# Kernel optimization log

Hardware: AMD Instinct MI355X
Metric: run time of the kernel (lower is better)

Reference implementation:

```python
import jax, jax.numpy as jnp
import numpy as np

L = 16384; ENC = 64; DMODEL = 256; DSTATE = 64; DCONV = 4; EXPAND = 2
NLAYERS = 3; NCLASSES = 11
DIN = EXPAND * DMODEL                 # 512
HEADDIM = 64
NHEADS = DIN // HEADDIM               # 8
DXBC = DIN + 2 * DSTATE               # 640 (ngroups=1)
DPROJ = 2 * DIN + 2 * DSTATE + NHEADS # 1160
NDIR = 6
ORDERS = [(0, 1, 2), (0, 2, 1), (1, 0, 2), (1, 2, 0), (2, 0, 1), (2, 1, 0)]
SCALES = [1, 2, 4]
EPS = 1e-5


def setup_inputs() -> dict:
    key = jax.random.key(0)
    ks = iter(jax.random.split(key, 64))
    def nrm(shape, s=0.02):
        return jax.random.normal(next(ks), shape, jnp.float32) * s
    S = len(SCALES)
    return {
        "vec_real": jax.random.normal(next(ks), (L, ENC), jnp.float32),
        "vec_imag": jax.random.normal(next(ks), (L, ENC), jnp.float32),
        "coords": jax.random.randint(next(ks), (L, 4), 0, 128, jnp.int32),
        # input projection (Linear 128->256, LayerNorm)
        "inp_w": nrm((2 * ENC, DMODEL)), "inp_b": jnp.zeros((DMODEL,)),
        "inp_ln_w": jnp.ones((DMODEL,)), "inp_ln_b": jnp.zeros((DMODEL,)),
        # shared Mamba2 blocks, stacked over NLAYERS
        "ln_w": jnp.ones((NLAYERS, DMODEL)), "ln_b": jnp.zeros((NLAYERS, DMODEL)),
        "in_proj_w": nrm((NLAYERS, DMODEL, DPROJ)),
        "conv_w": nrm((NLAYERS, DXBC, DCONV), 0.1), "conv_b": jnp.zeros((NLAYERS, DXBC)),
        "dt_bias": nrm((NLAYERS, NHEADS), 0.5),
        "A_log": jnp.log(jnp.broadcast_to(jnp.arange(1, NHEADS + 1, dtype=jnp.float32), (NLAYERS, NHEADS))),
        "Dskip": jnp.ones((NLAYERS, NHEADS)),
        "rms_w": jnp.ones((NLAYERS, DIN)),
        "out_proj_w": nrm((NLAYERS, DIN, DMODEL)),
        # fusion MLP
        "fus_ln_w": jnp.ones((NDIR * DMODEL,)), "fus_ln_b": jnp.zeros((NDIR * DMODEL,)),
        "fus_w": nrm((NDIR * DMODEL, DMODEL)), "fus_b": jnp.zeros((DMODEL,)),
        # classifier
        "cls_ln_w": jnp.ones((S * DMODEL,)), "cls_ln_b": jnp.zeros((S * DMODEL,)),
        "cls_w1": nrm((S * DMODEL, 2 * DMODEL)), "cls_b1": jnp.zeros((2 * DMODEL,)),
        "cls_w2": nrm((2 * DMODEL, DMODEL)), "cls_b2": jnp.zeros((DMODEL,)),
        "cls_w3": nrm((DMODEL, NCLASSES)), "cls_b3": jnp.zeros((NCLASSES,)),
    }


def layer_norm(x, w, b):
    mu = x.mean(-1, keepdims=True)
    v = ((x - mu) ** 2).mean(-1, keepdims=True)
    return (x - mu) * jax.lax.rsqrt(v + EPS) * w + b


def mamba2(x, in_proj_w, conv_w, conv_b, dt_bias, A_log, Dskip, rms_w, out_proj_w):
    # x: [B, L, DMODEL]
    Bsz, Ls, _ = x.shape
    zxbcdt = x @ in_proj_w                                  # [B,L,DPROJ]
    z, xBC, dt = jnp.split(zxbcdt, [DIN, DIN + DXBC], axis=-1)
    dt = jax.nn.softplus(dt + dt_bias)                      # [B,L,H]
    # causal depthwise conv1d over xBC, then SiLU
    xc = jnp.transpose(xBC, (0, 2, 1))                      # [B,C,L]
    xc = jax.lax.conv_general_dilated(xc, conv_w[:, None, :], (1,), [(DCONV - 1, 0)],
                                      feature_group_count=DXBC)
    xBC = jax.nn.silu(jnp.transpose(xc, (0, 2, 1)) + conv_b)
    xs, Bm, Cm = jnp.split(xBC, [DIN, DIN + DSTATE], axis=-1)
    xs = xs.reshape(Bsz, Ls, NHEADS, HEADDIM)               # [B,L,H,P]
    A = -jnp.exp(A_log)                                     # [H]

    def step(state, inp):
        x_t, B_t, C_t, dt_t = inp                           # [B,H,P],[B,S],[B,S],[B,H]
        dA = jnp.exp(dt_t * A)                              # [B,H]
        state = state * dA[..., None, None] + (dt_t[..., None, None]
                 * x_t[..., :, None] * B_t[:, None, None, :])
        y = jnp.einsum('bhps,bs->bhp', state, C_t)
        return state, y

    init = jnp.zeros((Bsz, NHEADS, HEADDIM, DSTATE), x.dtype)
    seq = (jnp.moveaxis(xs, 1, 0), jnp.moveaxis(Bm, 1, 0),
           jnp.moveaxis(Cm, 1, 0), jnp.moveaxis(dt, 1, 0))
    _, ys = jax.lax.scan(step, init, seq)                   # [L,B,H,P]
    y = jnp.moveaxis(ys, 0, 1) + Dskip[None, None, :, None] * xs
    y = y.reshape(Bsz, Ls, DIN)
    # gated RMSNorm (norm_before_gate=False)
    y = y * jax.nn.silu(z)
    y = y * jax.lax.rsqrt((y * y).mean(-1, keepdims=True) + EPS) * rms_w
    return y @ out_proj_w


def reference(vec_real, vec_imag, coords, inp_w, inp_b, inp_ln_w, inp_ln_b,
              ln_w, ln_b, in_proj_w, conv_w, conv_b, dt_bias, A_log, Dskip,
              rms_w, out_proj_w, fus_ln_w, fus_ln_b, fus_w, fus_b,
              cls_ln_w, cls_ln_b, cls_w1, cls_b1, cls_w2, cls_b2, cls_w3, cls_b3):
    x = jnp.concatenate([vec_real, vec_imag], -1)           # [L,128]
    h = layer_norm(x @ inp_w + inp_b, inp_ln_w, inp_ln_b)
    h = jax.nn.gelu(h, approximate=False)                   # [L,D]
    # 6 traversal orders via lexsort (np.lexsort semantics: last key primary)
    perms = [jnp.lexsort(tuple(coords[:, a] for a in reversed(axes))) for axes in ORDERS]
    perm = jnp.stack(perms)                                 # [6,L]
    inv = jnp.argsort(perm, axis=1)                         # [6,L]
    xs = h[perm]                                            # [6,L,D] (directions as batch, shared weights)

    def layer_step(xcur, p):
        lw, lb, ipw, cw, cb, dtb, al, dk, rw, ow = p
        y = mamba2(layer_norm(xcur, lw, lb), ipw, cw, cb, dtb, al, dk, rw, ow)
        return xcur + y, None

    params = (ln_w, ln_b, in_proj_w, conv_w, conv_b, dt_bias, A_log, Dskip, rms_w, out_proj_w)
    xs, _ = jax.lax.scan(layer_step, xs, params)
    restored = jnp.take_along_axis(xs, inv[:, :, None], axis=1)  # [6,L,D]
    multi = jnp.transpose(restored, (1, 0, 2)).reshape(L, NDIR * DMODEL)
    fused = layer_norm(multi, fus_ln_w, fus_ln_b) @ fus_w + fus_b
    fused = jax.nn.gelu(fused, approximate=False)           # [L,D]
    # multi-scale pooling; L divisible by every scale -> equal windows
    pooled = jnp.concatenate([fused.reshape(s, L // s, DMODEL).mean(1).mean(0)
                              for s in SCALES], 0)          # [3*D]
    hc = layer_norm(pooled, cls_ln_w, cls_ln_b)
    hc = jax.nn.gelu(hc @ cls_w1 + cls_b1, approximate=False)
    hc = jax.nn.gelu(hc @ cls_w2 + cls_b2, approximate=False)
    return hc @ cls_w3 + cls_b3                             # [NCLASSES]
```

## Files before the change

### kernel.cpp

```cpp
#include <hip/hip_runtime.h>
#include <hip/hip_bf16.h>
#include <math.h>

#define LSEQ 16384
#define NC 128

using short8  = __attribute__((ext_vector_type(8))) short;
using floatx4 = __attribute__((ext_vector_type(4))) float;

__device__ __forceinline__ float bf2f(ushort u){ union{unsigned u; float f;} x; x.u = ((unsigned)u)<<16; return x.f; }
__device__ __forceinline__ ushort f2bf(float f){ union{float f; unsigned u;} x; x.f=f; unsigned u=x.u; return (ushort)((u + 0x7FFFu + ((u>>16)&1u)) >> 16); }
__device__ __forceinline__ float geluf(float x){ return 0.5f*x*(1.f+erff(x*0.70710678118654752f)); }
__device__ __forceinline__ float siluf(float x){ return x/(1.f+__expf(-x)); }
__device__ __forceinline__ float softplusf(float x){ return x>20.f ? x : log1pf(__expf(x)); }

__device__ __forceinline__ float blockSum256(float v, float* red){
  int t = threadIdx.x;
  red[t]=v; __syncthreads();
  #pragma unroll
  for (int s=128;s>0;s>>=1){ if (t<s) red[t]+=red[t+s]; __syncthreads(); }
  float r = red[0]; __syncthreads();
  return r;
}

__device__ const int ORD[6][3] = {{0,1,2},{0,2,1},{1,0,2},{1,2,0},{2,0,1},{2,1,0}};

__global__ __launch_bounds__(256) void zrank_k(int* __restrict__ rank){
  rank[blockIdx.x*256 + threadIdx.x] = 0;
}

__global__ __launch_bounds__(256) void sortp_k(const int* __restrict__ coords, int* __restrict__ rank){
  __shared__ unsigned long long sk[256];
  int d = blockIdx.y; int tid = threadIdx.x;
  int a0=ORD[d][0], a1=ORD[d][1], a2=ORD[d][2];
  int ibase = blockIdx.x*1024;
  int jbase = blockIdx.z*4096;
  unsigned long long mykey[4]; int rk[4] = {0,0,0,0};
  #pragma unroll
  for (int r=0;r<4;++r){
    int i = ibase + r*256 + tid;
    unsigned k3 = ((unsigned)coords[i*4+a0]<<14) | ((unsigned)coords[i*4+a1]<<7) | (unsigned)coords[i*4+a2];
    mykey[r] = (((unsigned long long)k3)<<14) | (unsigned)i;
  }
  for (int j0=jbase; j0<jbase+4096; j0+=256){
    int j = j0 + tid;
    unsigned j3 = ((unsigned)coords[j*4+a0]<<14) | ((unsigned)coords[j*4+a1]<<7) | (unsigned)coords[j*4+a2];
    sk[tid] = (((unsigned long long)j3)<<14) | (unsigned)j;
    __syncthreads();
    #pragma unroll 8
    for (int jj=0; jj<256; ++jj){
      unsigned long long kj = sk[jj];
      #pragma unroll
      for (int r=0;r<4;++r) rk[r] += (kj < mykey[r]) ? 1 : 0;
    }
    __syncthreads();
  }
  #pragma unroll
  for (int r=0;r<4;++r)
    atomicAdd(&rank[d*LSEQ + ibase + r*256 + tid], rk[r]);
}

__global__ __launch_bounds__(256) void sfin_k(const int* __restrict__ rank, int* __restrict__ perm, int* __restrict__ inv){
  int g = blockIdx.x*256 + threadIdx.x;
  int d = g >> 14, i = g & 16383;
  int r = rank[g];
  perm[d*LSEQ + r] = i;
  inv[g] = r;
}

__global__ __launch_bounds__(256) void concat_k(const float* __restrict__ vr, const float* __restrict__ vi, float* __restrict__ xcat){
  int idx = blockIdx.x*256 + threadIdx.x;
  int i = idx >> 7, c = idx & 127;
  xcat[idx] = (c<64) ? vr[(i<<6)+c] : vi[(i<<6)+c-64];
}

__global__ __launch_bounds__(256) void tr_k(const float* __restrict__ in, ushort* __restrict__ out, int K, int N){
  __shared__ float tile[32][33];
  int tx = threadIdx.x & 31, ty = threadIdx.x >> 5;
  int k0 = blockIdx.y*32, n0 = blockIdx.x*32;
  #pragma unroll
  for (int q=0;q<4;++q){
    int k = k0 + ty + q*8, n = n0 + tx;
    if (k < K && n < N) tile[ty+q*8][tx] = in[(size_t)k*N + n];
  }
  __syncthreads();
  #pragma unroll
  for (int q=0;q<4;++q){
    int n = n0 + ty + q*8, k = k0 + tx;
    if (n < N && k < K) out[(size_t)n*K + k] = f2bf(tile[tx][ty+q*8]);
  }
}

template<int EPI, bool AF32>
__global__ __launch_bounds__(256) void gemm_bf_k(
  const void* __restrict__ Ain, int lda, const ushort* __restrict__ Bt,
  int N, int K, float* __restrict__ of,
  const float* __restrict__ bias, const float* __restrict__ rrow)
{
  __shared__ __align__(16) ushort As[64*32];
  __shared__ __align__(16) ushort Bs[64*32];
  int tid = threadIdx.x;
  int n0 = blockIdx.x*64, m0 = blockIdx.y*64;
  int w = tid>>6, lane = tid&63;
  int wm = (w>>1)*32, wn = (w&1)*32;
  int sr = tid>>2, skk = (tid&3)*8;
  floatx4 acc[2][2] = {};
  for (int k0=0; k0<K; k0+=32){
    if constexpr (AF32){
      const float* A = (const float*)Ain;
      float4 v0 = *(const float4*)(A + (size_t)(m0+sr)*lda + k0 + skk);
      float4 v1 = *(const float4*)(A + (size_t)(m0+sr)*lda + k0 + skk + 4);
      ushort o[8] = {f2bf(v0.x),f2bf(v0.y),f2bf(v0.z),f2bf(v0.w),f2bf(v1.x),f2bf(v1.y),f2bf(v1.z),f2bf(v1.w)};
      *(uint4*)(&As[sr*32+skk]) = *(uint4*)o;
    } else {
      const ushort* A = (const ushort*)Ain;
      *(uint4*)(&As[sr*32+skk]) = *(const uint4*)(A + (size_t)(m0+sr)*lda + k0 + skk);
    }
    uint4 bv = make_uint4(0u,0u,0u,0u);
    if (n0+sr < N) bv = *(const uint4*)(Bt + (size_t)(n0+sr)*K + k0 + skk);
    *(uint4*)(&Bs[sr*32+skk]) = bv;
    __syncthreads();
    int kq = lane>>4, l16 = lane&15;
    short8 bf0 = *(const short8*)(&Bs[(wn      + l16)*32 + kq*8]);
    short8 bf1 = *(const short8*)(&Bs[(wn + 16 + l16)*32 + kq*8]);
    #pragma unroll
    for (int ti=0; ti<2; ++ti){
      short8 af = *(const short8*)(&As[(wm + ti*16 + l16)*32 + kq*8]);
      acc[ti][0] = __builtin_amdgcn_mfma_f32_16x16x32_bf16(af, bf0, acc[ti][0], 0,0,0);
      acc[ti][1] = __builtin_amdgcn_mfma_f32_16x16x32_bf16(af, bf1, acc[ti][1], 0,0,0);
    }
    __syncthreads();
  }
  int l16 = lane&15, lq = lane>>4;
  #pragma unroll
  for (int ti=0; ti<2; ++ti)
  #pragma unroll
  for (int tj=0; tj<2; ++tj)
  #pragma unroll
  for (int r=0; r<4; ++r){
    int row = m0 + wm + ti*16 + lq*4 + r;
    int col = n0 + wn + tj*16 + l16;
    if (col >= N) continue;
    float v = acc[ti][tj][r];
    of[(size_t)row*N + col] = v + bias[col];
  }
}

template<int KC, int EPI>
__global__ __launch_bounds__(256) void gemmNS_k(
  const ushort* __restrict__ A, int lda, const ushort* __restrict__ Bt,
  float* __restrict__ of, const float* __restrict__ bias, const float* __restrict__ rrow)
{
  __shared__ __align__(16) ushort As[64*264];
  __shared__ __align__(16) ushort Bs[64*32];
  const int K = KC*256;
  int tid = threadIdx.x;
  int m0 = blockIdx.x*64;
  int w = tid>>6, lane = tid&63;
  int wm = (w>>1)*32, wn = (w&1)*32;
  int sr = tid>>2, skk = (tid&3)*8;
  int l16 = lane&15, kq = lane>>4;
  floatx4 acc[4][2][2] = {};
  for (int kb=0; kb<KC; ++kb){
    #pragma unroll
    for (int ki=0;ki<8;++ki)
      *(uint4*)(&As[sr*264 + ki*32 + skk]) = *(const uint4*)(A + (size_t)(m0+sr)*lda + kb*256 + ki*32 + skk);
    __syncthreads();
    for (int nt=0; nt<4; ++nt){
      for (int k0=0; k0<256; k0+=32){
        *(uint4*)(&Bs[sr*32+skk]) = *(const uint4*)(Bt + (size_t)(nt*64+sr)*K + kb*256 + k0 + skk);
        __syncthreads();
        short8 bf0 = *(const short8*)(&Bs[(wn      + l16)*32 + kq*8]);
        short8 bf1 = *(const short8*)(&Bs[(wn + 16 + l16)*32 + kq*8]);
        #pragma unroll
        for (int ti=0; ti<2; ++ti){
          short8 af = *(const short8*)(&As[(wm + ti*16 + l16)*264 + k0 + kq*8]);
          acc[nt][ti][0] = __builtin_amdgcn_mfma_f32_16x16x32_bf16(af, bf0, acc[nt][ti][0], 0,0,0);
          acc[nt][ti][1] = __builtin_amdgcn_mfma_f32_16x16x32_bf16(af, bf1, acc[nt][ti][1], 0,0,0);
        }
        __syncthreads();
      }
    }
  }
  #pragma unroll
  for (int nt=0; nt<4; ++nt)
  #pragma unroll
  for (int ti=0; ti<2; ++ti)
  #pragma unroll
  for (int tj=0; tj<2; ++tj)
  #pragma unroll
  for (int r=0; r<4; ++r){
    int row = m0 + wm + ti*16 + kq*4 + r;
    int col = nt*64 + wn + tj*16 + l16;
    float v = acc[nt][ti][tj][r];
    if (EPI==2) of[(size_t)row*256 + col] += v * rrow[row];
    else        of[(size_t)row*256 + col] = geluf(v + bias[col]);
  }
}

__global__ __launch_bounds__(256) void gemm1_k(
  const float* __restrict__ xs,
  const float* __restrict__ lnw, const float* __restrict__ lnb,
  const ushort* __restrict__ Wt,
  ushort* __restrict__ xbc, float* __restrict__ odt, const float* __restrict__ dtb)
{
  __shared__ __align__(16) ushort As[64*264];
  __shared__ __align__(16) ushort Bs[64*32];
  int tid = threadIdx.x;
  int m0 = blockIdx.x*64;
  int w = tid>>6, lane = tid&63;
  int wm = (w>>1)*32, wn = (w&1)*32;
  int sr = tid>>2, skk = (tid&3)*8;
  int l16 = lane&15, kq = lane>>4;
  float va[8][8];
  float s = 0.f, s2 = 0.f;
  const float* rowp = xs + (size_t)(m0+sr)*256;
  #pragma unroll
  for (int ki=0;ki<8;++ki){
    float4 v0 = *(const float4*)(rowp + ki*32 + skk);
    float4 v1 = *(const float4*)(rowp + ki*32 + skk + 4);
    va[ki][0]=v0.x; va[ki][1]=v0.y; va[ki][2]=v0.z; va[ki][3]=v0.w;
    va[ki][4]=v1.x; va[ki][5]=v1.y; va[ki][6]=v1.z; va[ki][7]=v1.w;
    #pragma unroll
    for (int j=0;j<8;++j){ s += va[ki][j]; s2 += va[ki][j]*va[ki][j]; }
  }
  s  += __shfl_xor(s,1,64);  s  += __shfl_xor(s,2,64);
  s2 += __shfl_xor(s2,1,64); s2 += __shfl_xor(s2,2,64);
  float mu = s*(1.f/256.f);
  float var = s2*(1.f/256.f) - mu*mu;
  float rs = rsqrtf(fmaxf(var,0.f)+1e-5f);
  #pragma unroll
  for (int ki=0;ki<8;++ki){
    ushort o[8];
    #pragma unroll
    for (int j=0;j<8;++j) o[j] = f2bf((va[ki][j]-mu)*rs*lnw[ki*32+skk+j] + lnb[ki*32+skk+j]);
    *(uint4*)(&As[sr*264 + ki*32 + skk]) = *(uint4*)o;
  }
  __syncthreads();
  for (int nt=0; nt<11; ++nt){
    floatx4 acc[2][2] = {};
    for (int k0=0; k0<256; k0+=32){
      int nr = 512 + nt*64 + sr;
      uint4 bv = make_uint4(0u,0u,0u,0u);
      if (nr < 1160) bv = *(const uint4*)(Wt + (size_t)nr*256 + k0 + skk);
      *(uint4*)(&Bs[sr*32+skk]) = bv;
      __syncthreads();
      short8 bf0 = *(const short8*)(&Bs[(wn      + l16)*32 + kq*8]);
      short8 bf1 = *(const short8*)(&Bs[(wn + 16 + l16)*32 + kq*8]);
      #pragma unroll
      for (int ti=0; ti<2; ++ti){
        short8 af = *(const short8*)(&As[(wm + ti*16 + l16)*264 + k0 + kq*8]);
        acc[ti][0] = __builtin_amdgcn_mfma_f32_16x16x32_bf16(af, bf0, acc[ti][0], 0,0,0);
        acc[ti][1] = __builtin_amdgcn_mfma_f32_16x16x32_bf16(af, bf1, acc[ti][1], 0,0,0);
      }
      __syncthreads();
    }
    #pragma unroll
    for (int ti=0; ti<2; ++ti)
    #pragma unroll
    for (int tj=0; tj<2; ++tj)
    #pragma unroll
    for (int r=0; r<4; ++r){
      int row = m0 + wm + ti*16 + kq*4 + r;
      int col = nt*64 + wn + tj*16 + l16;
      float v = acc[ti][tj][r];
      if (col < 640) xbc[(size_t)row*640 + col] = f2bf(v);
      else if (col < 648) odt[(size_t)row*8 + (col-640)] = softplusf(v + dtb[col-640]);
    }
  }
}

__global__ __launch_bounds__(256) void ln_gelu_k(const float* __restrict__ in, float* __restrict__ out,
    const float* __restrict__ w, const float* __restrict__ b){
  __shared__ float red[256];
  int t = threadIdx.x; size_t base = (size_t)blockIdx.x*256;
  float v = in[base+t];
  float mu = blockSum256(v, red) * (1.f/256.f);
  float dv = v - mu;
  float var = blockSum256(dv*dv, red) * (1.f/256.f);
  float rs = rsqrtf(var + 1e-5f);
  out[base+t] = geluf(dv*rs*w[t] + b[t]);
}

__global__ __launch_bounds__(256) void scatter_k(const float* __restrict__ h, const int* __restrict__ perm, float* __restrict__ xs){
  int blk = blockIdx.x;
  int t = threadIdx.x;
  int d = blk >> 14; int r = blk & 16383;
  int src = perm[d*LSEQ + r];
  xs[(size_t)blk*256 + t] = h[(size_t)src*256 + t];
}

__global__ __launch_bounds__(256) void bnd_k(const ushort* __restrict__ xbc, ushort* __restrict__ bnd){
  int b = blockIdx.x;
  int d = b / NC, c = b % NC;
  size_t row0 = (size_t)d*LSEQ + (size_t)c*128;
  for (int idx = threadIdx.x; idx < 3*640; idx += 256){
    int j = idx/640;
    ushort v = (c==0) ? (ushort)0 : xbc[(row0 - 3 + j)*640 + (idx - j*640)];
    bnd[(size_t)b*3*640 + idx] = v;
  }
}

__global__ __launch_bounds__(256) void conv_k(ushort* __restrict__ xbc, const ushort* __restrict__ bnd,
    const float* __restrict__ convw, const float* __restrict__ convb){
  int b = blockIdx.x;
  int d = b / NC, c = b % NC;
  size_t row0 = (size_t)d*LSEQ + (size_t)c*128;
  int tid = threadIdx.x;
  for (int s0 = tid; s0 < 640; s0 += 256){
    float w0=convw[s0*4], w1=convw[s0*4+1], w2=convw[s0*4+2], w3=convw[s0*4+3];
    float cb=convb[s0];
    float h0=0.f,h1=0.f,h2=0.f;
    if (c != 0){
      const ushort* bp = bnd + (size_t)b*3*640;
      h0=bf2f(bp[s0]); h1=bf2f(bp[640+s0]); h2=bf2f(bp[1280+s0]);
    }
    ushort* p = xbc + row0*640 + s0;
    for (int r=0;r<128;++r){
      float cur = bf2f(*p);
      *p = f2bf(siluf(cb + w0*h0 + w1*h1 + w2*h2 + w3*cur));
      h0=h1; h1=h2; h2=cur;
      p += 640;
    }
  }
}

__global__ __launch_bounds__(256) void ssd_dstate_k(
  const ushort* __restrict__ xbc, const float* __restrict__ dtf, const float* __restrict__ alog,
  ushort* __restrict__ dsb, float* __restrict__ gam, int dh0)
{
  int c = blockIdx.x, dhg = blockIdx.y;
  int dh = dh0 + dhg;
  int d = dh >> 3, h = dh & 7;
  int tid = threadIdx.x;
  float Ah = -__expf(alog[h]);
  __shared__ __align__(16) ushort XT[64*136];
  __shared__ __align__(16) ushort BwT[64*136];
  __shared__ float sdt[128];
  __shared__ float scs[128];
  size_t row0 = (size_t)d*LSEQ + (size_t)c*128;
  if (tid < 128){
    float v = dtf[(row0+tid)*8 + h];
    sdt[tid] = v;
    float x = v;
    #pragma unroll
    for (int o=1;o<64;o<<=1){ float t = __shfl_up(x,(unsigned)o,64); if ((tid&63)>=o) x += t; }
    scs[tid] = x;
  }
  __syncthreads();
  if (tid>=64 && tid<128) scs[tid] += scs[63];
  __syncthreads();
// ... 180 lines not shown
  }
  #pragma unroll
  for (int mt=0; mt<2; ++mt)
  #pragma unroll
  for (int nt=0; nt<4; ++nt)
  #pragma unroll
  for (int r=0; r<4; ++r){
    int tl = w*32 + mt*16 + kq*4 + r;
    int p  = nt*16 + l16;
    float xv = bf2f(XT[p*136 + tl]);
    float yv = Y[mt][nt][r] + Dv*xv;
    xbc[(row0 + tl)*640 + h*64 + p] = f2bf(yv);
  }
}

__global__ __launch_bounds__(512) void scan_legacy_k(ushort* __restrict__ xbc, const float* __restrict__ dtf,
  const float* __restrict__ convw, const float* __restrict__ convb,
  const float* __restrict__ alog, const float* __restrict__ dskip)
{
  int d = blockIdx.x >> 3, h = blockIdx.x & 7;
  int tid = threadIdx.x, p = tid & 63, sg = tid >> 6;
  float Ah = -__expf(alog[h]);
  float Dv = dskip[h];
  __shared__ float raw[19][192];
  __shared__ float cw[192][4];
  __shared__ float cb[192];
  __shared__ float sxc[16][192];
  __shared__ float sdt[16];
  __shared__ float sy[16][8][64];
  for (int c = tid; c < 192; c += 512){
    int ch = (c<64) ? h*64+c : (c<128 ? 512+(c-64) : 576+(c-128));
    #pragma unroll
    for (int k=0;k<4;++k) cw[c][k] = convw[ch*4+k];
    cb[c] = convb[ch];
  }
  for (int idx = tid; idx < 3*192; idx += 512) raw[idx/192][idx%192] = 0.f;
  float st[8];
  #pragma unroll
  for (int j=0;j<8;++j) st[j]=0.f;
  size_t rowbase = (size_t)d*LSEQ;
  __syncthreads();
  for (int t0=0; t0<LSEQ; t0+=16){
    for (int idx = tid; idx < 16*192; idx += 512){
      int tt = idx/192, c = idx%192;
      int ch = (c<64) ? h*64+c : (c<128 ? 512+(c-64) : 576+(c-128));
      raw[3+tt][c] = bf2f(xbc[(rowbase + t0 + tt)*640 + ch]);
    }
    if (tid < 16) sdt[tid] = dtf[(rowbase + t0 + tid)*8 + h];
    __syncthreads();
    for (int idx = tid; idx < 16*192; idx += 512){
      int tt = idx/192, c = idx%192;
      float v = cb[c] + cw[c][0]*raw[tt][c] + cw[c][1]*raw[tt+1][c]
                      + cw[c][2]*raw[tt+2][c] + cw[c][3]*raw[tt+3][c];
      sxc[tt][c] = siluf(v);
    }
    __syncthreads();
    for (int tt=0; tt<16; ++tt){
      float dtv = sdt[tt];
      float dA = __expf(dtv*Ah);
      float xb = dtv * sxc[tt][p];
      float Bl[8], Cl[8];
      #pragma unroll
      for (int q=0;q<2;++q){
        *(floatx4*)&Bl[q*4] = *(const floatx4*)&sxc[tt][64  + sg*8 + q*4];
        *(floatx4*)&Cl[q*4] = *(const floatx4*)&sxc[tt][128 + sg*8 + q*4];
      }
      float part = 0.f;
      #pragma unroll
      for (int j=0;j<8;++j){ st[j] = st[j]*dA + xb*Bl[j]; part += st[j]*Cl[j]; }
      sy[tt][sg][p] = part;
    }
    __syncthreads();
    for (int idx = tid; idx < 16*64; idx += 512){
      int tt = idx>>6, pp = idx&63;
      float yv = sy[tt][0][pp]+sy[tt][1][pp]+sy[tt][2][pp]+sy[tt][3][pp]
               + sy[tt][4][pp]+sy[tt][5][pp]+sy[tt][6][pp]+sy[tt][7][pp] + Dv*sxc[tt][pp];
      xbc[(rowbase + t0 + tt)*640 + h*64 + pp] = f2bf(yv);
    }
    for (int idx = tid; idx < 3*192; idx += 512){
      int r = idx/192, c = idx%192;
      raw[r][c] = raw[16+r][c];
    }
    __syncthreads();
  }
}

__global__ __launch_bounds__(256) void zgate_k(
  const float* __restrict__ xs,
  const float* __restrict__ lnw, const float* __restrict__ lnb,
  const ushort* __restrict__ Wzt, ushort* __restrict__ xbc,
  const float* __restrict__ rmsw, float* __restrict__ rrg)
{
  __shared__ __align__(16) ushort As[64*264];
  __shared__ __align__(16) ushort Bs[64*32];
  __shared__ float gsum[64*32];
  int tid = threadIdx.x;
  int m0 = blockIdx.x*64;
  int w = tid>>6, lane = tid&63;
  int wm = (w>>1)*32, wn = (w&1)*32;
  int sr = tid>>2, skk = (tid&3)*8;
  int l16 = lane&15, kq = lane>>4;
  float va[8][8];
  float s = 0.f, s2 = 0.f;
  const float* rowp = xs + (size_t)(m0+sr)*256;
  #pragma unroll
  for (int ki=0;ki<8;++ki){
    float4 v0 = *(const float4*)(rowp + ki*32 + skk);
    float4 v1 = *(const float4*)(rowp + ki*32 + skk + 4);
    va[ki][0]=v0.x; va[ki][1]=v0.y; va[ki][2]=v0.z; va[ki][3]=v0.w;
    va[ki][4]=v1.x; va[ki][5]=v1.y; va[ki][6]=v1.z; va[ki][7]=v1.w;
    #pragma unroll
    for (int j=0;j<8;++j){ s += va[ki][j]; s2 += va[ki][j]*va[ki][j]; }
  }
  s  += __shfl_xor(s,1,64);  s  += __shfl_xor(s,2,64);
  s2 += __shfl_xor(s2,1,64); s2 += __shfl_xor(s2,2,64);
  float mu = s*(1.f/256.f);
  float var = s2*(1.f/256.f) - mu*mu;
  float rs = rsqrtf(fmaxf(var,0.f)+1e-5f);
  #pragma unroll
  for (int ki=0;ki<8;++ki){
    ushort o[8];
    #pragma unroll
    for (int j=0;j<8;++j) o[j] = f2bf((va[ki][j]-mu)*rs*lnw[ki*32+skk+j] + lnb[ki*32+skk+j]);
    *(uint4*)(&As[sr*264 + ki*32 + skk]) = *(uint4*)o;
  }
  float racc[2][4] = {};
  __syncthreads();
  for (int nt=0; nt<8; ++nt){
    floatx4 acc[2][2] = {};
    for (int k0=0; k0<256; k0+=32){
      uint4 bv = *(const uint4*)(Wzt + (size_t)(nt*64 + sr)*256 + k0 + skk);
      *(uint4*)(&Bs[sr*32+skk]) = bv;
      __syncthreads();
      short8 bf0 = *(const short8*)(&Bs[(wn      + l16)*32 + kq*8]);
      short8 bf1 = *(const short8*)(&Bs[(wn + 16 + l16)*32 + kq*8]);
      #pragma unroll
      for (int ti=0; ti<2; ++ti){
        short8 af = *(const short8*)(&As[(wm + ti*16 + l16)*264 + k0 + kq*8]);
        acc[ti][0] = __builtin_amdgcn_mfma_f32_16x16x32_bf16(af, bf0, acc[ti][0], 0,0,0);
        acc[ti][1] = __builtin_amdgcn_mfma_f32_16x16x32_bf16(af, bf1, acc[ti][1], 0,0,0);
      }
      __syncthreads();
    }
    #pragma unroll
    for (int ti=0; ti<2; ++ti)
    #pragma unroll
    for (int tj=0; tj<2; ++tj)
    #pragma unroll
    for (int r=0; r<4; ++r){
      int row = m0 + wm + ti*16 + kq*4 + r;
      int col = nt*64 + wn + tj*16 + l16;
      float z = acc[ti][tj][r];
      float y = bf2f(xbc[(size_t)row*640 + col]);
      float g = y * siluf(z);
      racc[ti][r] += g*g;
      xbc[(size_t)row*640 + col] = f2bf(g * rmsw[col]);
    }
  }
  #pragma unroll
  for (int ti=0; ti<2; ++ti)
  #pragma unroll
  for (int r=0; r<4; ++r)
    gsum[(wm + ti*16 + kq*4 + r)*32 + (w&1)*16 + l16] = racc[ti][r];
  __syncthreads();
  if (tid < 64){
    float s0 = 0.f;
    #pragma unroll 8
    for (int cc=0;cc<32;++cc) s0 += gsum[tid*32+cc];
    rrg[m0+tid] = rsqrtf(s0*(1.f/512.f) + 1e-5f);
  }
}

__global__ __launch_bounds__(256) void fuse_ln_k(const float* __restrict__ xs, const int* __restrict__ inv,
    const float* __restrict__ w, const float* __restrict__ b, ushort* __restrict__ out){
  __shared__ float red[256];
  int i = blockIdx.x, t = threadIdx.x;
  float v[6];
  float s = 0.f;
  #pragma unroll
  for (int d=0; d<6; ++d){
    int r = inv[d*LSEQ + i];
    v[d] = xs[((size_t)d*LSEQ + r)*256 + t];
    s += v[d];
  }
  float mu = blockSum256(s, red) * (1.f/1536.f);
  float s2 = 0.f;
  #pragma unroll
  for (int d=0; d<6; ++d){ float dv = v[d]-mu; s2 += dv*dv; }
  float var = blockSum256(s2, red) * (1.f/1536.f);
  float rs = rsqrtf(var + 1e-5f);
  #pragma unroll
  for (int d=0; d<6; ++d){
    int c = d*256 + t;
    out[(size_t)i*1536 + c] = f2bf((v[d]-mu)*rs*w[c] + b[c]);
  }
}

__global__ void zero_k(float* p){ p[threadIdx.x] = 0.f; }

__global__ __launch_bounds__(256) void pool_k(const float* __restrict__ fused, float* __restrict__ pooled){
  int t = threadIdx.x;
  size_t r0 = (size_t)blockIdx.x*256;
  float s = 0.f;
  for (int r=0;r<256;++r) s += fused[(r0+r)*256 + t];
  atomicAdd(&pooled[t], s);
}

__global__ __launch_bounds__(256) void cls_k(const float* __restrict__ pooled,
  const float* __restrict__ lnw, const float* __restrict__ lnb,
  const float* __restrict__ w1, const float* __restrict__ b1,
  const float* __restrict__ w2, const float* __restrict__ b2,
  const float* __restrict__ w3, const float* __restrict__ b3, float* __restrict__ out)
{
  __shared__ float red[256];
  __shared__ float hcn[768]; __shared__ float h1[512]; __shared__ float h2[256];
  int t = threadIdx.x;
  float m = pooled[t] * (1.f/16384.f);
  float mu = blockSum256(m, red) * (1.f/256.f);
  float dv = m - mu;
  float var = blockSum256(dv*dv, red) * (1.f/256.f);
  float rs = rsqrtf(var + 1e-5f);
  #pragma unroll
  for (int rep=0; rep<3; ++rep){
    int c = rep*256 + t;
    hcn[c] = dv*rs*lnw[c] + lnb[c];
  }
  __syncthreads();
  for (int n=t; n<512; n+=256){
    float a = b1[n];
    for (int c=0;c<768;++c) a += hcn[c]*w1[c*512+n];
    h1[n] = geluf(a);
  }
  __syncthreads();
  {
    float a = b2[t];
    for (int c=0;c<512;++c) a += h1[c]*w2[c*256+t];
    h2[t] = geluf(a);
  }
  __syncthreads();
  if (t<11){
    float a = b3[t];
    for (int c=0;c<256;++c) a += h2[c]*w3[c*11+t];
    out[t] = a;
  }
}

extern "C" void kernel_launch(void* const* d_in, const int* in_sizes, int n_in,
                              void* d_out, int out_size, void* d_ws, size_t ws_size,
                              hipStream_t stream)
{
  const float* vec_real = (const float*)d_in[0];
  const float* vec_imag = (const float*)d_in[1];
  const int*   coords   = (const int*)d_in[2];
  const float* inp_w    = (const float*)d_in[3];
  const float* inp_b    = (const float*)d_in[4];
  const float* inp_ln_w = (const float*)d_in[5];
  const float* inp_ln_b = (const float*)d_in[6];
  const float* ln_w     = (const float*)d_in[7];
  const float* ln_b     = (const float*)d_in[8];
  const float* in_proj_w= (const float*)d_in[9];
  const float* conv_w   = (const float*)d_in[10];
  const float* conv_b   = (const float*)d_in[11];
  const float* dt_bias  = (const float*)d_in[12];
  const float* A_log    = (const float*)d_in[13];
  const float* Dskip    = (const float*)d_in[14];
  const float* rms_w    = (const float*)d_in[15];
  const float* out_proj_w=(const float*)d_in[16];
  const float* fus_ln_w = (const float*)d_in[17];
  const float* fus_ln_b = (const float*)d_in[18];
  const float* fus_w    = (const float*)d_in[19];
  const float* fus_b    = (const float*)d_in[20];
  const float* cls_ln_w = (const float*)d_in[21];
  const float* cls_ln_b = (const float*)d_in[22];
  const float* cls_w1   = (const float*)d_in[23];
  const float* cls_b1   = (const float*)d_in[24];
  const float* cls_w2   = (const float*)d_in[25];
  const float* cls_b2   = (const float*)d_in[26];
  const float* cls_w3   = (const float*)d_in[27];
  const float* cls_b3   = (const float*)d_in[28];
  (void)in_sizes; (void)n_in; (void)out_size;

  char* ws = (char*)d_ws;
  size_t off = 0;
  auto alloc = [&](size_t bytes)->char* { char* p = ws + off; off = (off + bytes + 255) & ~(size_t)255; return p; };
  int*    perm  = (int*)alloc((size_t)6*LSEQ*4);
  int*    inv   = (int*)alloc((size_t)6*LSEQ*4);
  float*  xs    = (float*)alloc((size_t)6*LSEQ*256*4);
  ushort* xbc   = (ushort*)alloc((size_t)6*LSEQ*640*2);
  float*  dtfb  = (float*)alloc((size_t)6*LSEQ*8*4);
  float*  rrg   = (float*)alloc((size_t)6*LSEQ*4);
  ushort* wtr   = (ushort*)alloc((size_t)1536*256*2);
  float*  pooled= (float*)alloc(256*4);
  size_t base_off = off;
  if (base_off > ws_size) return;

  float* gam = (float*)((char*)wtr + 600*1024);
  int* rankb = (int*)rrg;

  const size_t BND_SZ = (size_t)6*NC*3*640*2;
  size_t dsb_off = base_off + ((BND_SZ + 255) & ~(size_t)255);
  ushort* bndb = (ushort*)(ws + base_off);
  ushort* dsb  = (ushort*)(ws + dsb_off);
  long long avail2 = (long long)ws_size - (long long)dsb_off;
  int gsize = 0;
  const int cands[10] = {48,24,16,12,8,6,4,3,2,1};
  for (int ci=0; ci<10; ++ci){
    if ((long long)((size_t)cands[ci]*NC*4096*2 + 512) <= avail2){ gsize = cands[ci]; break; }
  }

  float*  xcat = (float*)((char*)xbc + 0);
  float*  tmpF = (float*)((char*)xbc + (16u<<20));
  float*  hbuf = (float*)((char*)xbc + (48u<<20));
  ushort* multiB = (ushort*)((char*)xbc + 0);
  float*  fused  = (float*)((char*)xbc + (100u<<20));

  dim3 b256(256);
  zrank_k<<<dim3(6*LSEQ/256),b256,0,stream>>>(rankb);
  sortp_k<<<dim3(16,6,4),b256,0,stream>>>(coords, rankb);
  sfin_k<<<dim3(6*LSEQ/256),b256,0,stream>>>(rankb, perm, inv);
  concat_k<<<dim3(LSEQ*128/256),b256,0,stream>>>(vec_real, vec_imag, xcat);
  tr_k<<<dim3(8,4),b256,0,stream>>>(inp_w, wtr, 128, 256);
  gemm_bf_k<0,true><<<dim3(4, LSEQ/64),b256,0,stream>>>(xcat, 128, wtr, 256, 128, tmpF, inp_b, nullptr);
  ln_gelu_k<<<dim3(LSEQ),b256,0,stream>>>(tmpF, hbuf, inp_ln_w, inp_ln_b);
  scatter_k<<<dim3(6*LSEQ),b256,0,stream>>>(hbuf, perm, xs);

  for (int l=0;l<3;++l){
    const float* cwp = conv_w + (size_t)l*640*4;
    const float* cbp = conv_b + (size_t)l*640;
    const float* alp = A_log + l*8;
    const float* dkp = Dskip + l*8;
    tr_k<<<dim3(37,8),b256,0,stream>>>(in_proj_w + (size_t)l*256*1160, wtr, 256, 1160);
    gemm1_k<<<dim3(6*LSEQ/64),b256,0,stream>>>(xs, ln_w + l*256, ln_b + l*256,
        wtr, xbc, dtfb, dt_bias + l*8);
    if (gsize > 0){
      bnd_k<<<dim3(6*NC),b256,0,stream>>>(xbc, bndb);
      conv_k<<<dim3(6*NC),b256,0,stream>>>(xbc, bndb, cwp, cbp);
      for (int dh0=0; dh0<48; dh0+=gsize){
        ssd_dstate_k<<<dim3(NC,gsize),b256,0,stream>>>(xbc, dtfb, alp, dsb, gam, dh0);
        ssd_scan_k<<<dim3(gsize,2),b256,0,stream>>>(dsb, gam, dh0);
        ssd_out_k<<<dim3(NC,gsize),b256,0,stream>>>(xbc, dsb, dtfb, alp, dkp, dh0);
      }
    } else {
      scan_legacy_k<<<dim3(48),dim3(512),0,stream>>>(xbc, dtfb, cwp, cbp, alp, dkp);
    }
    zgate_k<<<dim3(6*LSEQ/64),b256,0,stream>>>(xs, ln_w + l*256, ln_b + l*256,
        wtr, xbc, rms_w + l*512, rrg);
    tr_k<<<dim3(8,16),b256,0,stream>>>(out_proj_w + (size_t)l*512*256, wtr, 512, 256);
    gemmNS_k<2,2><<<dim3(6*LSEQ/64),b256,0,stream>>>(xbc, 640, wtr, xs, nullptr, rrg);
  }

  fuse_ln_k<<<dim3(LSEQ),b256,0,stream>>>(xs, inv, fus_ln_w, fus_ln_b, multiB);
  tr_k<<<dim3(8,48),b256,0,stream>>>(fus_w, wtr, 1536, 256);
  gemmNS_k<6,3><<<dim3(LSEQ/64),b256,0,stream>>>(multiB, 1536, wtr, fused, fus_b, nullptr);
  zero_k<<<dim3(1),b256,0,stream>>>(pooled);
  pool_k<<<dim3(64),b256,0,stream>>>(fused, pooled);
  cls_k<<<dim3(1),b256,0,stream>>>(pooled, cls_ln_w, cls_ln_b, cls_w1, cls_b1, cls_w2, cls_b2, cls_w3, cls_b3, (float*)d_out);
}
```

Baseline: 3.119 ms.

## Keep GEMM A operands in registers and load B directly, dropping LDS staging

The in_proj, z-gate and NS GEMM kernels now hold LayerNorm'd or bf16 A fragments in registers and read B fragments straight from global memory. This removes the LDS tiles and the per-k-step __syncthreads barriers. The sort-rank kernel's j-range is also split across twice as many blocks to expose more parallelism. The trade-off is higher register pressure and LayerNorm statistics recomputed per lane group, and B loads are no longer shared across waves through LDS, so they may not coalesce as well.

```diff
diff --git a/kernel.cpp b/kernel.cpp
--- a/kernel.cpp
+++ b/kernel.cpp
@@ -34,7 +34,7 @@
   int d = blockIdx.y; int tid = threadIdx.x;
   int a0=ORD[d][0], a1=ORD[d][1], a2=ORD[d][2];
   int ibase = blockIdx.x*1024;
-  int jbase = blockIdx.z*4096;
+  int jbase = blockIdx.z*2048;
   unsigned long long mykey[4]; int rk[4] = {0,0,0,0};
   #pragma unroll
   for (int r=0;r<4;++r){
@@ -42,7 +42,7 @@
     unsigned k3 = ((unsigned)coords[i*4+a0]<<14) | ((unsigned)coords[i*4+a1]<<7) | (unsigned)coords[i*4+a2];
     mykey[r] = (((unsigned long long)k3)<<14) | (unsigned)i;
   }
-  for (int j0=jbase; j0<jbase+4096; j0+=256){
+  for (int j0=jbase; j0<jbase+2048; j0+=256){
     int j = j0 + tid;
     unsigned j3 = ((unsigned)coords[j*4+a0]<<14) | ((unsigned)coords[j*4+a1]<<7) | (unsigned)coords[j*4+a2];
     sk[tid] = (((unsigned long long)j3)<<14) | (unsigned)j;
@@ -91,11 +91,9 @@
   }
 }
 
-template<int EPI, bool AF32>
-__global__ __launch_bounds__(256) void gemm_bf_k(
-  const void* __restrict__ Ain, int lda, const ushort* __restrict__ Bt,
-  int N, int K, float* __restrict__ of,
-  const float* __restrict__ bias, const float* __restrict__ rrow)
+__global__ __launch_bounds__(256) void gemm0_k(
+  const float* __restrict__ A, int lda, const ushort* __restrict__ Bt,
+  int N, int K, float* __restrict__ of, const float* __restrict__ bias)
 {
   __shared__ __align__(16) ushort As[64*32];
   __shared__ __align__(16) ushort Bs[64*32];
@@ -106,16 +104,10 @@
   int sr = tid>>2, skk = (tid&3)*8;
   floatx4 acc[2][2] = {};
   for (int k0=0; k0<K; k0+=32){
-    if constexpr (AF32){
-      const float* A = (const float*)Ain;
-      float4 v0 = *(const float4*)(A + (size_t)(m0+sr)*lda + k0 + skk);
-      float4 v1 = *(const float4*)(A + (size_t)(m0+sr)*lda + k0 + skk + 4);
-      ushort o[8] = {f2bf(v0.x),f2bf(v0.y),f2bf(v0.z),f2bf(v0.w),f2bf(v1.x),f2bf(v1.y),f2bf(v1.z),f2bf(v1.w)};
-      *(uint4*)(&As[sr*32+skk]) = *(uint4*)o;
-    } else {
-      const ushort* A = (const ushort*)Ain;
-      *(uint4*)(&As[sr*32+skk]) = *(const uint4*)(A + (size_t)(m0+sr)*lda + k0 + skk);
-    }
+    float4 v0 = *(const float4*)(A + (size_t)(m0+sr)*lda + k0 + skk);
+    float4 v1 = *(const float4*)(A + (size_t)(m0+sr)*lda + k0 + skk + 4);
+    ushort o[8] = {f2bf(v0.x),f2bf(v0.y),f2bf(v0.z),f2bf(v0.w),f2bf(v1.x),f2bf(v1.y),f2bf(v1.z),f2bf(v1.w)};
+    *(uint4*)(&As[sr*32+skk]) = *(uint4*)o;
     uint4 bv = make_uint4(0u,0u,0u,0u);
     if (n0+sr < N) bv = *(const uint4*)(Bt + (size_t)(n0+sr)*K + k0 + skk);
     *(uint4*)(&Bs[sr*32+skk]) = bv;
@@ -141,8 +133,142 @@
     int row = m0 + wm + ti*16 + lq*4 + r;
     int col = n0 + wn + tj*16 + l16;
     if (col >= N) continue;
-    float v = acc[ti][tj][r];
-    of[(size_t)row*N + col] = v + bias[col];
+    of[(size_t)row*N + col] = acc[ti][tj][r] + bias[col];
+  }
+}
+
+__device__ __forceinline__ void ln_frags(const float* __restrict__ xs, int row,
+    const float* __restrict__ lnw, const float* __restrict__ lnb, int kq, short8 afr[8])
+{
+  const float* rowp = xs + (size_t)row*256;
+  float v[64];
+  float s=0.f, s2=0.f;
+  #pragma unroll
+  for (int kc=0;kc<8;++kc){
+    float4 a0 = *(const float4*)(rowp + kc*32 + kq*8);
+    float4 a1 = *(const float4*)(rowp + kc*32 + kq*8 + 4);
+    v[kc*8+0]=a0.x; v[kc*8+1]=a0.y; v[kc*8+2]=a0.z; v[kc*8+3]=a0.w;
+    v[kc*8+4]=a1.x; v[kc*8+5]=a1.y; v[kc*8+6]=a1.z; v[kc*8+7]=a1.w;
+  }
+  #pragma unroll
+  for (int j=0;j<64;++j){ s += v[j]; s2 += v[j]*v[j]; }
+  s  += __shfl_xor(s,16,64);  s  += __shfl_xor(s,32,64);
+  s2 += __shfl_xor(s2,16,64); s2 += __shfl_xor(s2,32,64);
+  float mu = s*(1.f/256.f);
+  float var = s2*(1.f/256.f) - mu*mu;
+  float rs = rsqrtf(fmaxf(var,0.f)+1e-5f);
+  #pragma unroll
+  for (int kc=0;kc<8;++kc){
+    float4 w0 = *(const float4*)(lnw + kc*32 + kq*8);
+    float4 w1 = *(const float4*)(lnw + kc*32 + kq*8 + 4);
+    float4 b0 = *(const float4*)(lnb + kc*32 + kq*8);
+    float4 b1 = *(const float4*)(lnb + kc*32 + kq*8 + 4);
+    float wv[8] = {w0.x,w0.y,w0.z,w0.w,w1.x,w1.y,w1.z,w1.w};
+    float bv[8] = {b0.x,b0.y,b0.z,b0.w,b1.x,b1.y,b1.z,b1.w};
+    ushort o[8];
+    #pragma unroll
+    for (int j=0;j<8;++j) o[j] = f2bf((v[kc*8+j]-mu)*rs*wv[j] + bv[j]);
+    afr[kc] = *(short8*)o;
+  }
+}
+
+__global__ __launch_bounds__(256) void gemm1_k(
+  const float* __restrict__ xs,
+  const float* __restrict__ lnw, const float* __restrict__ lnb,
+  const ushort* __restrict__ Wt,
+  ushort* __restrict__ xbc, float* __restrict__ odt, const float* __restrict__ dtb)
+{
+  int tid = threadIdx.x;
+  int m0 = blockIdx.x*64;
+  int w = tid>>6, lane = tid&63;
+  int wm = (w>>1)*32, wn = (w&1)*32;
+  int l16 = lane&15, kq = lane>>4;
+  short8 afr[2][8];
+  ln_frags(xs, m0+wm+l16,    lnw, lnb, kq, afr[0]);
+  ln_frags(xs, m0+wm+16+l16, lnw, lnb, kq, afr[1]);
+  for (int nt=0; nt<11; ++nt){
+    floatx4 acc[2][2] = {};
+    #pragma unroll
+    for (int kc=0; kc<8; ++kc){
+      #pragma unroll
+      for (int tj=0; tj<2; ++tj){
+        int nr = 512 + nt*64 + wn + tj*16 + l16;
+        short8 bfr = {};
+        if (nr < 1160) bfr = *(const short8*)(Wt + (size_t)nr*256 + kc*32 + kq*8);
+        #pragma unroll
+        for (int mt=0; mt<2; ++mt)
+          acc[mt][tj] = __builtin_amdgcn_mfma_f32_16x16x32_bf16(afr[mt][kc], bfr, acc[mt][tj], 0,0,0);
+      }
+    }
+    #pragma unroll
+    for (int mt=0; mt<2; ++mt)
+    #pragma unroll
+    for (int tj=0; tj<2; ++tj)
+    #pragma unroll
+    for (int r=0; r<4; ++r){
+      int row = m0 + wm + mt*16 + kq*4 + r;
+      int col = nt*64 + wn + tj*16 + l16;
+      float v = acc[mt][tj][r];
+      if (col < 640) xbc[(size_t)row*640 + col] = f2bf(v);
+      else if (col < 648) odt[(size_t)row*8 + (col-640)] = softplusf(v + dtb[col-640]);
+    }
+  }
+}
+
+__global__ __launch_bounds__(256) void zgate_k(
+  const float* __restrict__ xs,
+  const float* __restrict__ lnw, const float* __restrict__ lnb,
+  const ushort* __restrict__ Wzt, ushort* __restrict__ xbc,
+  const float* __restrict__ rmsw, float* __restrict__ rrg)
+{
+  __shared__ float gsum[64*32];
+  int tid = threadIdx.x;
+  int m0 = blockIdx.x*64;
+  int w = tid>>6, lane = tid&63;
+  int wm = (w>>1)*32, wn = (w&1)*32;
+  int l16 = lane&15, kq = lane>>4;
+  short8 afr[2][8];
+  ln_frags(xs, m0+wm+l16,    lnw, lnb, kq, afr[0]);
+  ln_frags(xs, m0+wm+16+l16, lnw, lnb, kq, afr[1]);
+  float racc[2][4] = {};
+  for (int nt=0; nt<8; ++nt){
+    floatx4 acc[2][2] = {};
+    #pragma unroll
+    for (int kc=0; kc<8; ++kc){
+      #pragma unroll
+      for (int tj=0; tj<2; ++tj){
+        short8 bfr = *(const short8*)(Wzt + (size_t)(nt*64 + wn + tj*16 + l16)*256 + kc*32 + kq*8);
+        #pragma unroll
+        for (int mt=0; mt<2; ++mt)
+          acc[mt][tj] = __builtin_amdgcn_mfma_f32_16x16x32_bf16(afr[mt][kc], bfr, acc[mt][tj], 0,0,0);
+      }
+    }
+    #pragma unroll
+    for (int mt=0; mt<2; ++mt)
+    #pragma unroll
+    for (int tj=0; tj<2; ++tj)
+    #pragma unroll
+    for (int r=0; r<4; ++r){
+      int row = m0 + wm + mt*16 + kq*4 + r;
+      int col = nt*64 + wn + tj*16 + l16;
+      float z = acc[mt][tj][r];
+      float y = bf2f(xbc[(size_t)row*640 + col]);
+      float g = y * siluf(z);
+      racc[mt][r] += g*g;
+      xbc[(size_t)row*640 + col] = f2bf(g * rmsw[col]);
+    }
+  }
+  #pragma unroll
+  for (int mt=0; mt<2; ++mt)
+  #pragma unroll
+  for (int r=0; r<4; ++r)
+    gsum[(wm + mt*16 + kq*4 + r)*32 + (w&1)*16 + l16] = racc[mt][r];
+  __syncthreads();
+  if (tid < 64){
+    float s0 = 0.f;
+    #pragma unroll 8
+    for (int cc=0;cc<32;++cc) s0 += gsum[tid*32+cc];
+    rrg[m0+tid] = rsqrtf(s0*(1.f/512.f) + 1e-5f);
   }
 }
 
@@ -151,122 +277,48 @@
   const ushort* __restrict__ A, int lda, const ushort* __restrict__ Bt,
   float* __restrict__ of, const float* __restrict__ bias, const float* __restrict__ rrow)
 {
-  __shared__ __align__(16) ushort As[64*264];
-  __shared__ __align__(16) ushort Bs[64*32];
   const int K = KC*256;
   int tid = threadIdx.x;
   int m0 = blockIdx.x*64;
   int w = tid>>6, lane = tid&63;
   int wm = (w>>1)*32, wn = (w&1)*32;
-  int sr = tid>>2, skk = (tid&3)*8;
   int l16 = lane&15, kq = lane>>4;
   floatx4 acc[4][2][2] = {};
   for (int kb=0; kb<KC; ++kb){
-    #pragma unroll
-    for (int ki=0;ki<8;++ki)
-      *(uint4*)(&As[sr*264 + ki*32 + skk]) = *(const uint4*)(A + (size_t)(m0+sr)*lda + kb*256 + ki*32 + skk);
-    __syncthreads();
+    short8 afr[2][8];
+    #pragma unroll
+    for (int mt=0; mt<2; ++mt){
+      const ushort* rp = A + (size_t)(m0+wm+mt*16+l16)*lda + kb*256;
+      #pragma unroll
+      for (int kc=0; kc<8; ++kc) afr[mt][kc] = *(const short8*)(rp + kc*32 + kq*8);
+    }
+    #pragma unroll
     for (int nt=0; nt<4; ++nt){
-      for (int k0=0; k0<256; k0+=32){
-        *(uint4*)(&Bs[sr*32+skk]) = *(const uint4*)(Bt + (size_t)(nt*64+sr)*K + kb*256 + k0 + skk);
-        __syncthreads();
-        short8 bf0 = *(const short8*)(&Bs[(wn      + l16)*32 + kq*8]);
-        short8 bf1 = *(const short8*)(&Bs[(wn + 16 + l16)*32 + kq*8]);
+      #pragma unroll
+      for (int kc=0; kc<8; ++kc){
         #pragma unroll
-        for (int ti=0; ti<2; ++ti){
-          short8 af = *(const short8*)(&As[(wm + ti*16 + l16)*264 + k0 + kq*8]);
-          acc[nt][ti][0] = __builtin_amdgcn_mfma_f32_16x16x32_bf16(af, bf0, acc[nt][ti][0], 0,0,0);
-          acc[nt][ti][1] = __builtin_amdgcn_mfma_f32_16x16x32_bf16(af, bf1, acc[nt][ti][1], 0,0,0);
+        for (int tj=0; tj<2; ++tj){
+          short8 bfr = *(const short8*)(Bt + (size_t)(nt*64 + wn + tj*16 + l16)*K + kb*256 + kc*32 + kq*8);
+          #pragma unroll
+          for (int mt=0; mt<2; ++mt)
+            acc[nt][mt][tj] = __builtin_amdgcn_mfma_f32_16x16x32_bf16(afr[mt][kc], bfr, acc[nt][mt][tj], 0,0,0);
         }
-        __syncthreads();
       }
     }
   }
   #pragma unroll
   for (int nt=0; nt<4; ++nt)
   #pragma unroll
-  for (int ti=0; ti<2; ++ti)
+  for (int mt=0; mt<2; ++mt)
   #pragma unroll
   for (int tj=0; tj<2; ++tj)
   #pragma unroll
   for (int r=0; r<4; ++r){
-    int row = m0 + wm + ti*16 + kq*4 + r;
+    int row = m0 + wm + mt*16 + kq*4 + r;
     int col = nt*64 + wn + tj*16 + l16;
-    float v = acc[nt][ti][tj][r];
+    float v = acc[nt][mt][tj][r];
     if (EPI==2) of[(size_t)row*256 + col] += v * rrow[row];
     else        of[(size_t)row*256 + col] = geluf(v + bias[col]);
-  }
-}
-
-__global__ __launch_bounds__(256) void gemm1_k(
-  const float* __restrict__ xs,
-  const float* __restrict__ lnw, const float* __restrict__ lnb,
-  const ushort* __restrict__ Wt,
-  ushort* __restrict__ xbc, float* __restrict__ odt, const float* __restrict__ dtb)
-{
-  __shared__ __align__(16) ushort As[64*264];
-  __shared__ __align__(16) ushort Bs[64*32];
-  int tid = threadIdx.x;
-  int m0 = blockIdx.x*64;
-  int w = tid>>6, lane = tid&63;
-  int wm = (w>>1)*32, wn = (w&1)*32;
-  int sr = tid>>2, skk = (tid&3)*8;
-  int l16 = lane&15, kq = lane>>4;
-  float va[8][8];
-  float s = 0.f, s2 = 0.f;
-  const float* rowp = xs + (size_t)(m0+sr)*256;
-  #pragma unroll
-  for (int ki=0;ki<8;++ki){
-    float4 v0 = *(const float4*)(rowp + ki*32 + skk);
-    float4 v1 = *(const float4*)(rowp + ki*32 + skk + 4);
-    va[ki][0]=v0.x; va[ki][1]=v0.y; va[ki][2]=v0.z; va[ki][3]=v0.w;
-    va[ki][4]=v1.x; va[ki][5]=v1.y; va[ki][6]=v1.z; va[ki][7]=v1.w;
-    #pragma unroll
-    for (int j=0;j<8;++j){ s += va[ki][j]; s2 += va[ki][j]*va[ki][j]; }
-  }
-  s  += __shfl_xor(s,1,64);  s  += __shfl_xor(s,2,64);
-  s2 += __shfl_xor(s2,1,64); s2 += __shfl_xor(s2,2,64);
-  float mu = s*(1.f/256.f);
-  float var = s2*(1.f/256.f) - mu*mu;
-  float rs = rsqrtf(fmaxf(var,0.f)+1e-5f);
-  #pragma unroll
-  for (int ki=0;ki<8;++ki){
-    ushort o[8];
-    #pragma unroll
-    for (int j=0;j<8;++j) o[j] = f2bf((va[ki][j]-mu)*rs*lnw[ki*32+skk+j] + lnb[ki*32+skk+j]);
-    *(uint4*)(&As[sr*264 + ki*32 + skk]) = *(uint4*)o;
-  }
-  __syncthreads();
-  for (int nt=0; nt<11; ++nt){
-    floatx4 acc[2][2] = {};
-    for (int k0=0; k0<256; k0+=32){
-      int nr = 512 + nt*64 + sr;
-      uint4 bv = make_uint4(0u,0u,0u,0u);
-      if (nr < 1160) bv = *(const uint4*)(Wt + (size_t)nr*256 + k0 + skk);
-      *(uint4*)(&Bs[sr*32+skk]) = bv;
-      __syncthreads();
-      short8 bf0 = *(const short8*)(&Bs[(wn      + l16)*32 + kq*8]);
-      short8 bf1 = *(const short8*)(&Bs[(wn + 16 + l16)*32 + kq*8]);
-      #pragma unroll
-      for (int ti=0; ti<2; ++ti){
-        short8 af = *(const short8*)(&As[(wm + ti*16 + l16)*264 + k0 + kq*8]);
-        acc[ti][0] = __builtin_amdgcn_mfma_f32_16x16x32_bf16(af, bf0, acc[ti][0], 0,0,0);
-        acc[ti][1] = __builtin_amdgcn_mfma_f32_16x16x32_bf16(af, bf1, acc[ti][1], 0,0,0);
-      }
-      __syncthreads();
-    }
-    #pragma unroll
-    for (int ti=0; ti<2; ++ti)
-    #pragma unroll
-    for (int tj=0; tj<2; ++tj)
-    #pragma unroll
-    for (int r=0; r<4; ++r){
-      int row = m0 + wm + ti*16 + kq*4 + r;
-      int col = nt*64 + wn + tj*16 + l16;
-      float v = acc[ti][tj][r];
-      if (col < 640) xbc[(size_t)row*640 + col] = f2bf(v);
-      else if (col < 648) odt[(size_t)row*8 + (col-640)] = softplusf(v + dtb[col-640]);
-    }
   }
 }
 
@@ -613,92 +665,6 @@
       raw[r][c] = raw[16+r][c];
     }
     __syncthreads();
-  }
-}
-
-__global__ __launch_bounds__(256) void zgate_k(
-  const float* __restrict__ xs,
-  const float* __restrict__ lnw, const float* __restrict__ lnb,
-  const ushort* __restrict__ Wzt, ushort* __restrict__ xbc,
-  const float* __restrict__ rmsw, float* __restrict__ rrg)
-{
-  __shared__ __align__(16) ushort As[64*264];
-  __shared__ __align__(16) ushort Bs[64*32];
-  __shared__ float gsum[64*32];
-  int tid = threadIdx.x;
-  int m0 = blockIdx.x*64;
-  int w = tid>>6, lane = tid&63;
-  int wm = (w>>1)*32, wn = (w&1)*32;
-  int sr = tid>>2, skk = (tid&3)*8;
-  int l16 = lane&15, kq = lane>>4;
-  float va[8][8];
-  float s = 0.f, s2 = 0.f;
-  const float* rowp = xs + (size_t)(m0+sr)*256;
-  #pragma unroll
-  for (int ki=0;ki<8;++ki){
-    float4 v0 = *(const float4*)(rowp + ki*32 + skk);
-    float4 v1 = *(const float4*)(rowp + ki*32 + skk + 4);
-    va[ki][0]=v0.x; va[ki][1]=v0.y; va[ki][2]=v0.z; va[ki][3]=v0.w;
-    va[ki][4]=v1.x; va[ki][5]=v1.y; va[ki][6]=v1.z; va[ki][7]=v1.w;
-    #pragma unroll
-    for (int j=0;j<8;++j){ s += va[ki][j]; s2 += va[ki][j]*va[ki][j]; }
-  }
-  s  += __shfl_xor(s,1,64);  s  += __shfl_xor(s,2,64);
-  s2 += __shfl_xor(s2,1,64); s2 += __shfl_xor(s2,2,64);
-  float mu = s*(1.f/256.f);
-  float var = s2*(1.f/256.f) - mu*mu;
-  float rs = rsqrtf(fmaxf(var,0.f)+1e-5f);
-  #pragma unroll
-  for (int ki=0;ki<8;++ki){
-    ushort o[8];
-    #pragma unroll
-    for (int j=0;j<8;++j) o[j] = f2bf((va[ki][j]-mu)*rs*lnw[ki*32+skk+j] + lnb[ki*32+skk+j]);
-    *(uint4*)(&As[sr*264 + ki*32 + skk]) = *(uint4*)o;
-  }
-  float racc[2][4] = {};
-  __syncthreads();
-  for (int nt=0; nt<8; ++nt){
-    floatx4 acc[2][2] = {};
-    for (int k0=0; k0<256; k0+=32){
-      uint4 bv = *(const uint4*)(Wzt + (size_t)(nt*64 + sr)*256 + k0 + skk);
-      *(uint4*)(&Bs[sr*32+skk]) = bv;
-      __syncthreads();
-      short8 bf0 = *(const short8*)(&Bs[(wn      + l16)*32 + kq*8]);
-      short8 bf1 = *(const short8*)(&Bs[(wn + 16 + l16)*32 + kq*8]);
-      #pragma unroll
-      for (int ti=0; ti<2; ++ti){
-        short8 af = *(const short8*)(&As[(wm + ti*16 + l16)*264 + k0 + kq*8]);
-        acc[ti][0] = __builtin_amdgcn_mfma_f32_16x16x32_bf16(af, bf0, acc[ti][0], 0,0,0);
-        acc[ti][1] = __builtin_amdgcn_mfma_f32_16x16x32_bf16(af, bf1, acc[ti][1], 0,0,0);
-      }
-      __syncthreads();
-    }
-    #pragma unroll
-    for (int ti=0; ti<2; ++ti)
-    #pragma unroll
-    for (int tj=0; tj<2; ++tj)
-    #pragma unroll
-    for (int r=0; r<4; ++r){
-      int row = m0 + wm + ti*16 + kq*4 + r;
-      int col = nt*64 + wn + tj*16 + l16;
-      float z = acc[ti][tj][r];
-      float y = bf2f(xbc[(size_t)row*640 + col]);
-      float g = y * siluf(z);
-      racc[ti][r] += g*g;
-      xbc[(size_t)row*640 + col] = f2bf(g * rmsw[col]);
-    }
-  }
-  #pragma unroll
-  for (int ti=0; ti<2; ++ti)
-  #pragma unroll
-  for (int r=0; r<4; ++r)
-    gsum[(wm + ti*16 + kq*4 + r)*32 + (w&1)*16 + l16] = racc[ti][r];
-  __syncthreads();
-  if (tid < 64){
-    float s0 = 0.f;
-    #pragma unroll 8
-    for (int cc=0;cc<32;++cc) s0 += gsum[tid*32+cc];
-    rrg[m0+tid] = rsqrtf(s0*(1.f/512.f) + 1e-5f);
   }
 }
 
@@ -847,11 +813,11 @@
 
   dim3 b256(256);
   zrank_k<<<dim3(6*LSEQ/256),b256,0,stream>>>(rankb);
-  sortp_k<<<dim3(16,6,4),b256,0,stream>>>(coords, rankb);
+  sortp_k<<<dim3(16,6,8),b256,0,stream>>>(coords, rankb);
   sfin_k<<<dim3(6*LSEQ/256),b256,0,stream>>>(rankb, perm, inv);
   concat_k<<<dim3(LSEQ*128/256),b256,0,stream>>>(vec_real, vec_imag, xcat);
   tr_k<<<dim3(8,4),b256,0,stream>>>(inp_w, wtr, 128, 256);
-  gemm_bf_k<0,true><<<dim3(4, LSEQ/64),b256,0,stream>>>(xcat, 128, wtr, 256, 128, tmpF, inp_b, nullptr);
+  gemm0_k<<<dim3(4, LSEQ/64),b256,0,stream>>>(xcat, 128, wtr, 256, 128, tmpF, inp_b);
   ln_gelu_k<<<dim3(LSEQ),b256,0,stream>>>(tmpF, hbuf, inp_ln_w, inp_ln_b);
   scatter_k<<<dim3(6*LSEQ),b256,0,stream>>>(hbuf, perm, xs);
 
```

Measured after the change: 3.477 ms. +11.5%, slower.
